# Optimization experiments

Measured on AMD Instinct MI355X. Metric: run time of the kernel, lower is better.

## Reference

```python
import jax, jax.numpy as jnp
import numpy as np

DIM = 256
HEADS = 4
DIM_HEAD = 32
HIDDEN = HEADS * DIM_HEAD  # 128
GROUPS = min(DIM // 4, 32)  # 32
H = W = 256
EPS = 1e-5


def setup_inputs() -> dict:
    key = jax.random.key(0)
    ks = jax.random.split(key, 5)
    scale = 0.02
    return {
        "x": jax.random.normal(ks[0], (DIM, H, W), dtype=jnp.float32),
        "gn_weight": jnp.ones((DIM,), dtype=jnp.float32),
        "gn_bias": jnp.zeros((DIM,), dtype=jnp.float32),
        "qkv_weight": jax.random.normal(ks[1], (3 * HIDDEN, DIM), dtype=jnp.float32) * scale,
        "qkv_bias": jax.random.normal(ks[2], (3 * HIDDEN,), dtype=jnp.float32) * scale,
        "out_weight": jax.random.normal(ks[3], (DIM, HIDDEN), dtype=jnp.float32) * scale,
        "out_bias": jax.random.normal(ks[4], (DIM,), dtype=jnp.float32) * scale,
    }


def reference(x, gn_weight, gn_bias, qkv_weight, qkv_bias, out_weight, out_bias):
    c, h, w = x.shape  # (256, 256, 256)
    n = h * w

    # GroupNorm: stats per group over (channels_in_group * spatial)
    xg = x.reshape(GROUPS, -1)
    mean = jnp.mean(xg, axis=1, keepdims=True)
    var = jnp.var(xg, axis=1, keepdims=True)
    xn = ((xg - mean) * jax.lax.rsqrt(var + EPS)).reshape(c, h, w)
    xn = xn * gn_weight[:, None, None] + gn_bias[:, None, None]

    # 1x1 QKV conv -> (3*heads*dim_head, h, w), then split per rearrange layout
    qkv = jnp.einsum('oc,chw->ohw', qkv_weight, xn) + qkv_bias[:, None, None]
    qkv = qkv.reshape(3, HEADS, DIM_HEAD, n)
    q, k, v = qkv[0], qkv[1], qkv[2]

    # linear attention: softmax over spatial positions of k
    k = jax.nn.softmax(k, axis=-1)
    context = jnp.einsum('hdn,hen->hde', k, v)   # (heads, d, d) tiny
    out = jnp.einsum('hde,hdn->hen', context, q)  # (heads, d, n)
    out = out.reshape(HIDDEN, h, w)

    # 1x1 output conv
    return jnp.einsum('oc,chw->ohw', out_weight, out) + out_bias[:, None, None]
```

## Files before the change

kernel.cpp:

```cpp
#include <hip/hip_runtime.h>
#include <stdint.h>

typedef float f32x4 __attribute__((ext_vector_type(4)));
typedef short short8 __attribute__((ext_vector_type(8)));
typedef short short4v __attribute__((ext_vector_type(4)));

#define N_SPATIAL 65536
#define DIM 256
#define GROUPS 32
#define HIDDEN 128

__device__ __forceinline__ float b2f(uint16_t u) {
  union { uint32_t u; float f; } v; v.u = ((uint32_t)u) << 16; return v.f;
}
__device__ __forceinline__ uint16_t f2b(float f) {
  union { float f; uint32_t u; } v; v.f = f;
  uint32_t r = (v.u + 0x7FFFu + ((v.u >> 16) & 1u)) >> 16;
  return (uint16_t)r;
}

__device__ __forceinline__ void async16(const void* g, void* l) {
  __builtin_amdgcn_global_load_lds(
      (__attribute__((address_space(1))) void*)g,
      (__attribute__((address_space(3))) void*)l, 16, 0, 0);
}

__global__ __launch_bounds__(256) void k1_transpose_stats(
    const float* __restrict__ x, uint16_t* __restrict__ xT, float* __restrict__ gnp) {
  __shared__ uint16_t xs[64][264];
  const int t = threadIdx.x;
  const int n0 = blockIdx.x * 64;
  const int c_l = (t >> 2) & 15;
  const int nq  = (t & 3) + 4 * (t >> 6);
  for (int p = 0; p < 16; ++p) {
    int c = 16 * p + c_l;
    float4 v = *(const float4*)(x + (size_t)c * N_SPATIAL + n0 + nq * 4);
    int nn = nq * 4;
    xs[nn + 0][c] = f2b(v.x); xs[nn + 1][c] = f2b(v.y);
    xs[nn + 2][c] = f2b(v.z); xs[nn + 3][c] = f2b(v.w);
  }
  __syncthreads();
  {
    int g = t >> 3; int c = g * 8 + (t & 7);
    float s = 0.f, ss = 0.f;
    for (int n = 0; n < 64; ++n) { float f = b2f(xs[n][c]); s += f; ss += f * f; }
    s  += __shfl_xor(s, 1, 64);  ss += __shfl_xor(ss, 1, 64);
    s  += __shfl_xor(s, 2, 64);  ss += __shfl_xor(ss, 2, 64);
    s  += __shfl_xor(s, 4, 64);  ss += __shfl_xor(ss, 4, 64);
    if ((t & 7) == 0) {
      gnp[((size_t)blockIdx.x * 32 + g) * 2 + 0] = s;
      gnp[((size_t)blockIdx.x * 32 + g) * 2 + 1] = ss;
    }
  }
  for (int p = 0; p < 8; ++p) {
    int j = t + 256 * p; int n = j >> 5; int c16 = j & 31;
    f32x4 val = *(const f32x4*)((const char*)&xs[0][0] + n * 528 + c16 * 16);
    *(f32x4*)((char*)xT + ((size_t)(n0 + n)) * 512 + c16 * 16) = val;
  }
}

__global__ __launch_bounds__(256) void k2f_fold(
    const float* __restrict__ gnp, const float* __restrict__ gnw,
    const float* __restrict__ gnb, const float* __restrict__ qw,
    const float* __restrict__ qb, uint16_t* __restrict__ wp,
    float* __restrict__ biasp) {
  __shared__ float sred[4][32];
  __shared__ float ssred[4][32];
  __shared__ float sa[256], sb[256];
  __shared__ float rbias[4];
  const int o = blockIdx.x; const int t = threadIdx.x;
  const int g = t & 31, slice = t >> 5;
  float s = 0.f, ss = 0.f;
  for (int i = 0; i < 128; ++i) {
    int c = slice * 128 + i;
    s  += gnp[((size_t)c * 32 + g) * 2 + 0];
    ss += gnp[((size_t)c * 32 + g) * 2 + 1];
  }
  s += __shfl_xor(s, 32, 64); ss += __shfl_xor(ss, 32, 64);
  const int wv = t >> 6;
  if ((t & 63) < 32) { sred[wv][g] = s; ssred[wv][g] = ss; }
  __syncthreads();
  if (t < 32) {
    float S  = sred[0][t] + sred[1][t] + sred[2][t] + sred[3][t];
    float SS = ssred[0][t] + ssred[1][t] + ssred[2][t] + ssred[3][t];
    const float invN = 1.0f / 524288.0f;
    float mean = S * invN;
    float var  = SS * invN - mean * mean;
    float rs   = rsqrtf(var + 1e-5f);
    sred[0][t] = mean; ssred[0][t] = rs;
  }
  __syncthreads();
  {
    int gg = t >> 3;
    float aa = gnw[t] * ssred[0][gg];
    sa[t] = aa;
    sb[t] = gnb[t] - sred[0][gg] * aa;
  }
  __syncthreads();
  float w = qw[(size_t)o * 256 + t];
  wp[(size_t)o * 256 + t] = f2b(w * sa[t]);
  float p = w * sb[t];
  for (int m = 32; m >= 1; m >>= 1) p += __shfl_xor(p, m, 64);
  if ((t & 63) == 0) rbias[t >> 6] = p;
  __syncthreads();
  if (t == 0) biasp[o] = qb[o] + rbias[0] + rbias[1] + rbias[2] + rbias[3];
}

__global__ __launch_bounds__(256) void k3_kv(
    const uint16_t* __restrict__ xT, const uint16_t* __restrict__ wp,
    const float* __restrict__ biasp, float* __restrict__ part) {
  __shared__ __align__(16) char smem[40960];
  const int t = threadIdx.x;
  const int l = t & 63, wid = t >> 6;
  const int lrow = l & 15, lk = l >> 4;

  const int n0 = blockIdx.x * 64;
  f32x4 acc[4][4] = {};
  for (int ks = 0; ks < 4; ++ks) {
    const int k0 = ks * 64;
    __syncthreads();
    #pragma unroll
    for (int it = 0; it < 8; ++it) {
      int s = it * 256 + t;
      int row = s >> 3, c = s & 7;
      const char* gsrc = (const char*)wp + (size_t)(128 + row) * 512 + k0 * 2 + ((c ^ (row & 7)) << 4);
      async16(gsrc, smem + (s & ~63) * 16);
    }
    #pragma unroll
    for (int it = 0; it < 2; ++it) {
      int s = it * 256 + t;
      int row = s >> 3, c = s & 7;
      const char* gsrc = (const char*)xT + (size_t)(n0 + row) * 512 + k0 * 2 + ((c ^ (row & 7)) << 4);
      async16(gsrc, smem + 32768 + (s & ~63) * 16);
    }
    __syncthreads();
    #pragma unroll
    for (int kk = 0; kk < 2; ++kk) {
      short8 a[4], b[4];
      #pragma unroll
      for (int m = 0; m < 4; ++m) {
        int row = wid * 64 + m * 16 + lrow;
        a[m] = *(const short8*)(&smem[row * 128 + (((kk * 4 + lk) ^ (row & 7)) << 4)]);
      }
      #pragma unroll
      for (int n = 0; n < 4; ++n) {
        int row = n * 16 + lrow;
        b[n] = *(const short8*)(&smem[32768 + row * 128 + (((kk * 4 + lk) ^ (row & 7)) << 4)]);
      }
      #pragma unroll
      for (int m = 0; m < 4; ++m)
        #pragma unroll
        for (int n = 0; n < 4; ++n)
          acc[m][n] = __builtin_amdgcn_mfma_f32_16x16x32_bf16(a[m], b[n], acc[m][n], 0, 0, 0);
    }
  }
  __syncthreads();

  float denp[16];
  #pragma unroll
  for (int i = 0; i < 16; ++i) denp[i] = 0.f;
  {
    const bool isk = wid < 2;
    const int base = isk ? 0 : 16384;
    #pragma unroll
    for (int m = 0; m < 4; ++m) {
      float bb[4];
      #pragma unroll
      for (int j = 0; j < 4; ++j) bb[j] = biasp[128 + wid * 64 + m * 16 + lk * 4 + j];
      #pragma unroll
      for (int n = 0; n < 4; ++n) {
        int col = n * 16 + lrow;
        int coff = col >> 3, cbyte = (col & 7) * 2;
        #pragma unroll
        for (int j = 0; j < 4; ++j) {
          int rloc = ((wid * 64) & 127) + m * 16 + lk * 4 + j;
          float val = acc[m][n][j] + bb[j];
          if (isk) { val = __expf(val); denp[m * 4 + j] += val; }
          *(uint16_t*)(&smem[base + rloc * 128 + ((coff ^ (rloc & 7)) << 4) + cbyte]) = f2b(val);
        }
      }
    }
  }
  __syncthreads();

  f32x4 cacc[2][2] = {};
  {
    const int h = wid;
    #pragma unroll
    for (int kw = 0; kw < 2; ++kw) {
      short8 ae[2], be[2];
      #pragma unroll
      for (int mf = 0; mf < 2; ++mf) {
        int row = h * 32 + mf * 16 + lrow;
        ae[mf] = *(const short8*)(&smem[row * 128 + (((kw * 4 + lk) ^ (row & 7)) << 4)]);
      }
      #pragma unroll
      for (int nf = 0; nf < 2; ++nf) {
        int row = h * 32 + nf * 16 + lrow;
        be[nf] = *(const short8*)(&smem[16384 + row * 128 + (((kw * 4 + lk) ^ (row & 7)) << 4)]);
      }
      #pragma unroll
      for (int mf = 0; mf < 2; ++mf)
        #pragma unroll
        for (int nf = 0; nf < 2; ++nf)
          cacc[mf][nf] = __builtin_amdgcn_mfma_f32_16x16x32_bf16(ae[mf], be[nf], cacc[mf][nf], 0, 0, 0);
    }
  }
  float* pp = part + (size_t)blockIdx.x * 4224;
  {
    float* ph = pp + wid * 1056;
    #pragma unroll
    for (int mf = 0; mf < 2; ++mf)
      #pragma unroll
      for (int nf = 0; nf < 2; ++nf)
        #pragma unroll
        for (int j = 0; j < 4; ++j) {
          int d = mf * 16 + lk * 4 + j, e = nf * 16 + lrow;
          ph[d * 32 + e] = cacc[mf][nf][j];
        }
  }
  if (wid < 2) {
    #pragma unroll
    for (int i = 0; i < 16; ++i) {
      denp[i] += __shfl_xor(denp[i], 1, 64);
      denp[i] += __shfl_xor(denp[i], 2, 64);
      denp[i] += __shfl_xor(denp[i], 4, 64);
      denp[i] += __shfl_xor(denp[i], 8, 64);
    }
    if (lrow == 0) {
      #pragma unroll
      for (int m = 0; m < 4; ++m)
        #pragma unroll
        for (int j = 0; j < 4; ++j) {
          int r = wid * 64 + m * 16 + lk * 4 + j;
          pp[(r >> 5) * 1056 + 1024 + (r & 31)] = denp[m * 4 + j];
        }
    }
  }
}

__global__ __launch_bounds__(256) void k6_reduce(
    const float* __restrict__ part, float* __restrict__ part2) {
  const int bx = blockIdx.x;
  const int idb = bx % 17, cg = bx / 17;
  const int id = idb * 256 + threadIdx.x;
  if (id >= 4224) return;
  const float* p = part + (size_t)cg * 128 * 4224 + id;
  float s0 = 0.f, s1 = 0.f, s2 = 0.f, s3 = 0.f;
  for (int c = 0; c < 128; c += 4) {
    s0 += p[(size_t)(c + 0) * 4224];
    s1 += p[(size_t)(c + 1) * 4224];
    s2 += p[(size_t)(c + 2) * 4224];
    s3 += p[(size_t)(c + 3) * 4224];
  }
  part2[cg * 4224 + id] = (s0 + s1) + (s2 + s3);
}

__global__ __launch_bounds__(256) void kM_fold(
    const float* __restrict__ ow, const float* __restrict__ part2,
    const uint16_t* __restrict__ wp, const float* __restrict__ biasp,
    const float* __restrict__ ob, uint16_t* __restrict__ M2,
    float* __restrict__ bias2) {
  __shared__ float sctx[4224];
  __shared__ float sow[128];
  __shared__ float smrow[128];
  __shared__ float rb[4];
  const int o = blockIdx.x; const int t = threadIdx.x;
  for (int i = t; i < 4224; i += 256) {
    float s = 0.f;
    #pragma unroll
    for (int g = 0; g < 8; ++g) s += part2[g * 4224 + i];
    sctx[i] = s;
  }
  if (t < 128) sow[t] = ow[(size_t)o * 128 + t];
  __syncthreads();
  if (t < 128) {
    int h = t >> 5, d = t & 31;
    const float* cs = sctx + h * 1056;
    float den = cs[1024 + d];
    float s = 0.f;
    #pragma unroll
    for (int e = 0; e < 32; ++e) {
      int er = (e + d) & 31;
      s += sow[h * 32 + er] * cs[d * 32 + er];
    }
    smrow[t] = s / den;
  }
  __syncthreads();
  float acc = 0.f;
  for (int d = 0; d < 128; ++d) acc += smrow[d] * b2f(wp[(size_t)d * 256 + t]);
  M2[(size_t)o * 256 + t] = f2b(acc);
  float p = (t < 128) ? smrow[t] * biasp[t] : 0.f;
  for (int m = 32; m >= 1; m >>= 1) p += __shfl_xor(p, m, 64);
  if ((t & 63) == 0) rb[t >> 6] = p;
  __syncthreads();
  if (t == 0) bias2[o] = ob[o] + rb[0] + rb[1] + rb[2] + rb[3];
}

__global__ __launch_bounds__(256) void k7_out(
    const uint16_t* __restrict__ xT, const uint16_t* __restrict__ M2,
    const float* __restrict__ bias2, float* __restrict__ out) {
  __shared__ __align__(16) char smem[32768];
  const int t = threadIdx.x;
  const int mt = blockIdx.x & 1, nt = blockIdx.x >> 1;
  const int o0 = mt * 128, n0 = nt * 128;
  const int l = t & 63, wid = t >> 6, wr = wid >> 1, wc = wid & 1;
  const int lrow = l & 15, lk = l >> 4;

  f32x4 acc[4][4] = {};
  for (int ks = 0; ks < 4; ++ks) {
    const int k0 = ks * 64;
    __syncthreads();
    #pragma unroll
    for (int it = 0; it < 4; ++it) {
      int s = it * 256 + t;
      int row = s >> 3, c = s & 7;
      const char* gsrc = (const char*)M2 + (size_t)(o0 + row) * 512 + k0 * 2 + ((c ^ (row & 7)) << 4);
      async16(gsrc, smem + (s & ~63) * 16);
    }
    #pragma unroll
    for (int it = 0; it < 4; ++it) {
      int s = it * 256 + t;
      int row = s >> 3, c = s & 7;
      const char* gsrc = (const char*)xT + (size_t)(n0 + row) * 512 + k0 * 2 + ((c ^ (row & 7)) << 4);
      async16(gsrc, smem + 16384 + (s & ~63) * 16);
    }
    __syncthreads();
    #pragma unroll
    for (int kk = 0; kk < 2; ++kk) {
      short8 a[4], b[4];
      #pragma unroll
      for (int m = 0; m < 4; ++m) {
        int row = wr * 64 + m * 16 + lrow;
        a[m] = *(const short8*)(&smem[row * 128 + (((kk * 4 + lk) ^ (row & 7)) << 4)]);
      }
      #pragma unroll
      for (int n = 0; n < 4; ++n) {
        int row = wc * 64 + n * 16 + lrow;
        b[n] = *(const short8*)(&smem[16384 + row * 128 + (((kk * 4 + lk) ^ (row & 7)) << 4)]);
      }
      #pragma unroll
      for (int m = 0; m < 4; ++m)
        #pragma unroll
        for (int n = 0; n < 4; ++n)
          acc[m][n] = __builtin_amdgcn_mfma_f32_16x16x32_bf16(a[m], b[n], acc[m][n], 0, 0, 0);
    }
  }

  #pragma unroll
  for (int half = 0; half < 2; ++half) {
    __syncthreads();
    if (wr == half) {
      #pragma unroll
      for (int m = 0; m < 4; ++m) {
        int rb = m * 16 + lk * 4;
        float bb[4];
        #pragma unroll
        for (int j = 0; j < 4; ++j) bb[j] = bias2[o0 + half * 64 + rb + j];
        #pragma unroll
        for (int n = 0; n < 4; ++n) {
          int col = wc * 64 + n * 16 + lrow;
          #pragma unroll
          for (int j = 0; j < 4; ++j) {
            int row = rb + j;
            *(float*)(&smem[row * 512 + ((((col >> 2) ^ (row & 7)) << 4)) + (col & 3) * 4]) =
                acc[m][n][j] + bb[j];
          }
        }
      }
    }
    __syncthreads();
    #pragma unroll
    for (int p = 0; p < 8; ++p) {
      int flat = t + 256 * p; int row = flat >> 5, c = flat & 31;
      f32x4 v = *(const f32x4*)(&smem[row * 512 + (((c ^ (row & 7)) << 4))]);
      *(f32x4*)(out + (size_t)(o0 + half * 64 + row) * N_SPATIAL + n0 + c * 4) = v;
    }
  }
}

extern "C" void kernel_launch(void* const* d_in, const int* in_sizes, int n_in,
                              void* d_out, int out_size, void* d_ws, size_t ws_size,
                              hipStream_t stream) {
  const float* x   = (const float*)d_in[0];
  const float* gnw = (const float*)d_in[1];
  const float* gnb = (const float*)d_in[2];
  const float* qw  = (const float*)d_in[3];
  const float* qb  = (const float*)d_in[4];
  const float* ow  = (const float*)d_in[5];
  const float* ob  = (const float*)d_in[6];
  float* out = (float*)d_out;
  char* ws = (char*)d_ws;

  uint16_t* xT    = (uint16_t*)(ws + 0);
  uint16_t* wp    = (uint16_t*)(ws + 33554432);
  float*    biasp = (float*)   (ws + 33751040);
  float*    gnp   = (float*)   (ws + 33752576);
  float*    part  = (float*)   (ws + 34014720);
  float*    part2 = (float*)   (ws + 51316224);
  uint16_t* M2    = (uint16_t*)(ws + 51451392);
  float*    bias2 = (float*)   (ws + 51582464);

  k1_transpose_stats<<<dim3(1024), dim3(256), 0, stream>>>(x, xT, gnp);
  k2f_fold<<<dim3(384), dim3(256), 0, stream>>>(gnp, gnw, gnb, qw, qb, wp, biasp);
  k3_kv<<<dim3(1024), dim3(256), 0, stream>>>(xT, wp, biasp, part);
  k6_reduce<<<dim3(136), dim3(256), 0, stream>>>(part, part2);
  kM_fold<<<dim3(256), dim3(256), 0, stream>>>(ow, part2, wp, biasp, ob, M2, bias2);
  k7_out<<<dim3(1024), dim3(256), 0, stream>>>(xT, M2, bias2, out);
}
```

Measured before the change: 92.46 us.

## Split GroupNorm fold into stats and weight kernels, store kv partials as bf16

The GroupNorm fold kernel is split in two. A 32-block kernel computes per-channel scale and shift once, and a light 64-thread kernel folds them into the QKV weights, so the old 384 blocks no longer each redo the full statistics reduction. The per-block context partials written by k3_kv are now stored as bf16 instead of fp32, halving the traffic of that write and of the k6_reduce read. Occupancy hints (launch_bounds min 4 blocks) are added to k3_kv and k7_out. The cost is an extra launch and some precision loss in the summed partials.

```diff
diff --git a/kernel.cpp b/kernel.cpp
--- a/kernel.cpp
+++ b/kernel.cpp
@@ -6,9 +6,6 @@
 typedef short short4v __attribute__((ext_vector_type(4)));
 
 #define N_SPATIAL 65536
-#define DIM 256
-#define GROUPS 32
-#define HIDDEN 128
 
 __device__ __forceinline__ float b2f(uint16_t u) {
   union { uint32_t u; float f; } v; v.u = ((uint32_t)u) << 16; return v.f;
@@ -59,56 +56,54 @@
   }
 }
 
-__global__ __launch_bounds__(256) void k2f_fold(
+__global__ __launch_bounds__(256) void k2_stats_final(
     const float* __restrict__ gnp, const float* __restrict__ gnw,
-    const float* __restrict__ gnb, const float* __restrict__ qw,
-    const float* __restrict__ qb, uint16_t* __restrict__ wp,
-    float* __restrict__ biasp) {
-  __shared__ float sred[4][32];
-  __shared__ float ssred[4][32];
-  __shared__ float sa[256], sb[256];
-  __shared__ float rbias[4];
-  const int o = blockIdx.x; const int t = threadIdx.x;
-  const int g = t & 31, slice = t >> 5;
+    const float* __restrict__ gnb, float* __restrict__ ab) {
+  __shared__ float red[4][2];
+  const int g = blockIdx.x; const int t = threadIdx.x;
   float s = 0.f, ss = 0.f;
-  for (int i = 0; i < 128; ++i) {
-    int c = slice * 128 + i;
+  for (int c = t; c < 1024; c += 256) {
     s  += gnp[((size_t)c * 32 + g) * 2 + 0];
     ss += gnp[((size_t)c * 32 + g) * 2 + 1];
   }
-  s += __shfl_xor(s, 32, 64); ss += __shfl_xor(ss, 32, 64);
-  const int wv = t >> 6;
-  if ((t & 63) < 32) { sred[wv][g] = s; ssred[wv][g] = ss; }
-  __syncthreads();
-  if (t < 32) {
-    float S  = sred[0][t] + sred[1][t] + sred[2][t] + sred[3][t];
-    float SS = ssred[0][t] + ssred[1][t] + ssred[2][t] + ssred[3][t];
+  for (int m = 32; m >= 1; m >>= 1) { s += __shfl_xor(s, m, 64); ss += __shfl_xor(ss, m, 64); }
+  if ((t & 63) == 0) { red[t >> 6][0] = s; red[t >> 6][1] = ss; }
+  __syncthreads();
+  if (t == 0) {
+    float S  = red[0][0] + red[1][0] + red[2][0] + red[3][0];
+    float SS = red[0][1] + red[1][1] + red[2][1] + red[3][1];
     const float invN = 1.0f / 524288.0f;
     float mean = S * invN;
     float var  = SS * invN - mean * mean;
     float rs   = rsqrtf(var + 1e-5f);
-    sred[0][t] = mean; ssred[0][t] = rs;
-  }
-  __syncthreads();
-  {
-    int gg = t >> 3;
-    float aa = gnw[t] * ssred[0][gg];
-    sa[t] = aa;
-    sb[t] = gnb[t] - sred[0][gg] * aa;
-  }
-  __syncthreads();
-  float w = qw[(size_t)o * 256 + t];
-  wp[(size_t)o * 256 + t] = f2b(w * sa[t]);
-  float p = w * sb[t];
-  for (int m = 32; m >= 1; m >>= 1) p += __shfl_xor(p, m, 64);
-  if ((t & 63) == 0) rbias[t >> 6] = p;
-  __syncthreads();
-  if (t == 0) biasp[o] = qb[o] + rbias[0] + rbias[1] + rbias[2] + rbias[3];
-}
-
-__global__ __launch_bounds__(256) void k3_kv(
+    for (int i = 0; i < 8; ++i) {
+      int c = g * 8 + i;
+      float aa = gnw[c] * rs;
+      ab[c] = aa;
+      ab[256 + c] = gnb[c] - mean * aa;
+    }
+  }
+}
+
+__global__ __launch_bounds__(64) void k2b_fold_w(
+    const float* __restrict__ qw, const float* __restrict__ qb,
+    const float* __restrict__ ab, uint16_t* __restrict__ wp, float* __restrict__ biasp) {
+  const int o = blockIdx.x; const int l = threadIdx.x;
+  float4 w  = *(const float4*)(qw + (size_t)o * 256 + l * 4);
+  float4 av = *(const float4*)(ab + l * 4);
+  float4 bv = *(const float4*)(ab + 256 + l * 4);
+  short4v pk;
+  pk[0] = (short)f2b(w.x * av.x); pk[1] = (short)f2b(w.y * av.y);
+  pk[2] = (short)f2b(w.z * av.z); pk[3] = (short)f2b(w.w * av.w);
+  *(short4v*)(wp + (size_t)o * 256 + l * 4) = pk;
+  float part = w.x * bv.x + w.y * bv.y + w.z * bv.z + w.w * bv.w;
+  for (int m = 32; m >= 1; m >>= 1) part += __shfl_xor(part, m, 64);
+  if (l == 0) biasp[o] = qb[o] + part;
+}
+
+__global__ __launch_bounds__(256, 4) void k3_kv(
     const uint16_t* __restrict__ xT, const uint16_t* __restrict__ wp,
-    const float* __restrict__ biasp, float* __restrict__ part) {
+    const float* __restrict__ biasp, uint16_t* __restrict__ part) {
   __shared__ __align__(16) char smem[40960];
   const int t = threadIdx.x;
   const int l = t & 63, wid = t >> 6;
@@ -206,9 +201,9 @@
           cacc[mf][nf] = __builtin_amdgcn_mfma_f32_16x16x32_bf16(ae[mf], be[nf], cacc[mf][nf], 0, 0, 0);
     }
   }
-  float* pp = part + (size_t)blockIdx.x * 4224;
+  uint16_t* pp = part + (size_t)blockIdx.x * 4224;
   {
-    float* ph = pp + wid * 1056;
+    uint16_t* ph = pp + wid * 1056;
     #pragma unroll
     for (int mf = 0; mf < 2; ++mf)
       #pragma unroll
@@ -216,7 +211,7 @@
         #pragma unroll
         for (int j = 0; j < 4; ++j) {
           int d = mf * 16 + lk * 4 + j, e = nf * 16 + lrow;
-          ph[d * 32 + e] = cacc[mf][nf][j];
+          ph[d * 32 + e] = f2b(cacc[mf][nf][j]);
         }
   }
   if (wid < 2) {
@@ -233,25 +228,25 @@
         #pragma unroll
         for (int j = 0; j < 4; ++j) {
           int r = wid * 64 + m * 16 + lk * 4 + j;
-          pp[(r >> 5) * 1056 + 1024 + (r & 31)] = denp[m * 4 + j];
+          pp[(r >> 5) * 1056 + 1024 + (r & 31)] = f2b(denp[m * 4 + j]);
         }
     }
   }
 }
 
 __global__ __launch_bounds__(256) void k6_reduce(
-    const float* __restrict__ part, float* __restrict__ part2) {
+    const uint16_t* __restrict__ part, float* __restrict__ part2) {
   const int bx = blockIdx.x;
   const int idb = bx % 17, cg = bx / 17;
   const int id = idb * 256 + threadIdx.x;
   if (id >= 4224) return;
-  const float* p = part + (size_t)cg * 128 * 4224 + id;
+  const uint16_t* p = part + (size_t)cg * 128 * 4224 + id;
   float s0 = 0.f, s1 = 0.f, s2 = 0.f, s3 = 0.f;
   for (int c = 0; c < 128; c += 4) {
-    s0 += p[(size_t)(c + 0) * 4224];
-    s1 += p[(size_t)(c + 1) * 4224];
-    s2 += p[(size_t)(c + 2) * 4224];
-    s3 += p[(size_t)(c + 3) * 4224];
+    s0 += b2f(p[(size_t)(c + 0) * 4224]);
+    s1 += b2f(p[(size_t)(c + 1) * 4224]);
+    s2 += b2f(p[(size_t)(c + 2) * 4224]);
+    s3 += b2f(p[(size_t)(c + 3) * 4224]);
   }
   part2[cg * 4224 + id] = (s0 + s1) + (s2 + s3);
 }
@@ -297,7 +292,7 @@
   if (t == 0) bias2[o] = ob[o] + rb[0] + rb[1] + rb[2] + rb[3];
 }
 
-__global__ __launch_bounds__(256) void k7_out(
+__global__ __launch_bounds__(256, 4) void k7_out(
     const uint16_t* __restrict__ xT, const uint16_t* __restrict__ M2,
     const float* __restrict__ bias2, float* __restrict__ out) {
   __shared__ __align__(16) char smem[32768];
@@ -395,14 +390,16 @@
   uint16_t* xT    = (uint16_t*)(ws + 0);
   uint16_t* wp    = (uint16_t*)(ws + 33554432);
   float*    biasp = (float*)   (ws + 33751040);
-  float*    gnp   = (float*)   (ws + 33752576);
-  float*    part  = (float*)   (ws + 34014720);
-  float*    part2 = (float*)   (ws + 51316224);
-  uint16_t* M2    = (uint16_t*)(ws + 51451392);
-  float*    bias2 = (float*)   (ws + 51582464);
+  float*    ab    = (float*)   (ws + 33753088);
+  float*    gnp   = (float*)   (ws + 33755136);
+  uint16_t* part  = (uint16_t*)(ws + 34017280);
+  float*    part2 = (float*)   (ws + 42668032);
+  uint16_t* M2    = (uint16_t*)(ws + 42803200);
+  float*    bias2 = (float*)   (ws + 42934272);
 
   k1_transpose_stats<<<dim3(1024), dim3(256), 0, stream>>>(x, xT, gnp);
-  k2f_fold<<<dim3(384), dim3(256), 0, stream>>>(gnp, gnw, gnb, qw, qb, wp, biasp);
+  k2_stats_final<<<dim3(32), dim3(256), 0, stream>>>(gnp, gnw, gnb, ab);
+  k2b_fold_w<<<dim3(384), dim3(64), 0, stream>>>(qw, qb, ab, wp, biasp);
   k3_kv<<<dim3(1024), dim3(256), 0, stream>>>(xT, wp, biasp, part);
   k6_reduce<<<dim3(136), dim3(256), 0, stream>>>(part, part2);
   kM_fold<<<dim3(256), dim3(256), 0, stream>>>(ow, part2, wp, biasp, ob, M2, bias2);
```

Measured after the change: 83.40 us. 1.11x faster.
